# Kernel tuning notes

Measured on AMD Instinct MI355X. Metric: run time of the kernel, lower is better.

The kernel has to match this reference:

```python
import jax, jax.numpy as jnp
import numpy as np

NUM_HEADS = 8


def setup_inputs() -> dict:
    key = jax.random.key(0)
    ks = jax.random.split(key, 9)
    B, C, H, W = 2, 64, 48, 48
    Ck, Cv, Co = 64, 64, 64
    s = lambda fan_in: 1.0 / np.sqrt(fan_in)
    return {
        "x": jax.random.normal(ks[0], (B, C, H, W), jnp.float32),
        "Wq": jax.random.normal(ks[1], (Ck, C), jnp.float32) * s(C),
        "bq": jnp.zeros((Ck,), jnp.float32),
        "Wk": jax.random.normal(ks[2], (Ck, C), jnp.float32) * s(C),
        "bk": jnp.zeros((Ck,), jnp.float32),
        "Wv": jax.random.normal(ks[3], (Cv, C), jnp.float32) * s(C),
        "bv": jnp.zeros((Cv,), jnp.float32),
        "Wo": jax.random.normal(ks[4], (Co, Cv), jnp.float32) * s(Cv),
        "bo": jnp.zeros((Co,), jnp.float32),
    }


def _conv1x1(x, W, b):
    # 1x1 conv == channel matmul: [B,C,H,W] x [O,C] -> [B,O,H,W]
    return jnp.einsum("oc,bchw->bohw", W, x) + b[None, :, None, None]


def reference(x, Wq, bq, Wk, bk, Wv, bv, Wo, bo):
    B, _, H, W_ = x.shape
    nh = NUM_HEADS
    Ck, Cv = Wq.shape[0], Wv.shape[0]
    d = Ck // nh
    L = H * W_

    # NOTE: original torch code scales q in place via a view, so returned q is scaled.
    q = _conv1x1(x, Wq, bq) * (d ** -0.5)
    k = _conv1x1(x, Wk, bk)
    v = _conv1x1(x, Wv, bv)

    qs = q.reshape(B, nh, d, L)          # [B,h,d,Lq]
    ks = k.reshape(B, nh, d, L)          # [B,h,d,Lk]
    vs = v.reshape(B, nh, Cv // nh, L)   # [B,h,dv,Lk]

    logits = jnp.einsum("bhdq,bhdk->bhqk", qs, ks)   # [B,h,Lq,Lk]
    # softmax over the QUERY axis (dim=2), as in the original nn.Softmax(dim=2)
    weights = jax.nn.softmax(logits, axis=2)
    o = jnp.einsum("bhck,bhqk->bhcq", vs, weights)   # [B,h,dv,Lq]

    o = o.reshape(B, Cv, H, W_)
    out = _conv1x1(o, Wo, bo)
    return out, q
```

## Files before the change

kernel.cpp:

```cpp
#include <hip/hip_runtime.h>

#define LL   2304
#define CCH  64
#define NHD  8

static constexpr float QSCALE = 0.35355339059327373f;
static constexpr float LOG2E  = 1.4426950408889634f;

typedef _Float16 half2_t  __attribute__((ext_vector_type(2)));
typedef _Float16 half4_t  __attribute__((ext_vector_type(4)));
typedef _Float16 half8_t  __attribute__((ext_vector_type(8)));
typedef float    float16_t __attribute__((ext_vector_type(16)));

__device__ __forceinline__ half2_t pk_f16(float a, float b) {
    return __builtin_bit_cast(half2_t, __builtin_amdgcn_cvt_pkrtz(a, b));
}


__global__ __launch_bounds__(256) void k_qkv(
    const float* __restrict__ x,
    const float* __restrict__ Wq, const float* __restrict__ bq,
    const float* __restrict__ Wk, const float* __restrict__ bk,
    const float* __restrict__ Wv, const float* __restrict__ bv,
    float* __restrict__ qout,
    _Float16* __restrict__ Qt, _Float16* __restrict__ Kt, _Float16* __restrict__ Vt)
{
    __shared__ float xs[64][32];
    __shared__ float wsm[64][64];
    const int t   = threadIdx.x;
    const int l0  = blockIdx.x * 32;
    const int b   = blockIdx.y;
    const int mat = blockIdx.z;
    const float* W    = (mat == 0) ? Wq : (mat == 1 ? Wk : Wv);
    const float* bias = (mat == 0) ? bq : (mat == 1 ? bk : bv);
    const float* xb = x + (long)b * CCH * LL;

    #pragma unroll
    for (int p = 0; p < 2; ++p) {
        int flat = (p * 256 + t) * 4;
        int c = flat >> 5, l = flat & 31;
        *(float4*)&xs[c][l] = *(const float4*)&xb[(long)c * LL + l0 + l];
    }
    #pragma unroll
    for (int p = 0; p < 4; ++p) {
        int flat = (p * 256 + t) * 4;
        int c = flat >> 6, l = flat & 63;
        *(float4*)&wsm[c][l] = *(const float4*)&W[flat];
    }
    __syncthreads();

    const int l  = t & 31;
    const int cg = t >> 5;
    float acc[8];
    #pragma unroll
    for (int j = 0; j < 8; ++j) acc[j] = 0.f;
    for (int cp = 0; cp < 64; ++cp) {
        float xv = xs[cp][l];
        #pragma unroll
        for (int j = 0; j < 8; ++j) acc[j] = fmaf(wsm[cg * 8 + j][cp], xv, acc[j]);
    }
    long row = (long)(b * NHD + cg) * LL + l0 + l;
    if (mat == 0) {
        half8_t pq;
        #pragma unroll
        for (int j = 0; j < 8; ++j) {
            float qv = (acc[j] + bias[cg * 8 + j]) * QSCALE;
            qout[((long)b * CCH + cg * 8 + j) * LL + l0 + l] = qv;
            pq[j] = (_Float16)(qv * LOG2E);
        }
        *(half8_t*)(Qt + row * 8) = pq;
    } else if (mat == 1) {
        half8_t pk;
        #pragma unroll
        for (int j = 0; j < 8; ++j) pk[j] = (_Float16)(acc[j] + bias[cg * 8 + j]);
        *(half8_t*)(Kt + row * 8) = pk;
    } else {
        half8_t pv;
        #pragma unroll
        for (int j = 0; j < 8; ++j) pv[j] = (_Float16)(acc[j] + bias[cg * 8 + j]);
        *(half8_t*)(Vt + row * 8) = pv;
    }
}

__global__ __launch_bounds__(256) void k_denom(
    const _Float16* __restrict__ Qt, const _Float16* __restrict__ Kt,
    const _Float16* __restrict__ Vt, _Float16* __restrict__ V2)
{
    __shared__ _Float16 lQ[2][2][256][4];
    __shared__ float Dp[4][32];
    __shared__ float rDs[32];
    const int t    = threadIdx.x;
    const int bh   = blockIdx.y;
    const int k0   = blockIdx.x * 32;
    const int lane = t & 63, w = t >> 6;
    const int half = lane >> 5, l31 = lane & 31;

    half4_t kA = *(const half4_t*)(Kt + ((long)bh * LL + k0 + l31) * 8 + half * 4);

    const float4* qbase = (const float4*)(Qt + (long)bh * LL * 8);
    float4 pre = qbase[t];
    *(float2*)&lQ[0][0][t][0] = make_float2(pre.x, pre.y);
    *(float2*)&lQ[0][1][t][0] = make_float2(pre.z, pre.w);
    __syncthreads();

    float16_t D0 = {}, D1 = {};
    for (int ch = 0; ch < 9; ++ch) {
        const int buf = ch & 1;
        if (ch + 1 < 9) pre = qbase[(ch + 1) * 256 + t];
        {
            half4_t qB = *(const half4_t*)&lQ[buf][half][(2 * w + 0) * 32 + l31][0];
            float16_t S = __builtin_amdgcn_mfma_f32_32x32x8f16(kA, qB, (float16_t){}, 0, 0, 0);
            #pragma unroll
            for (int r = 0; r < 16; ++r) D0[r] += __builtin_amdgcn_exp2f(S[r]);
        }
        {
            half4_t qB = *(const half4_t*)&lQ[buf][half][(2 * w + 1) * 32 + l31][0];
            float16_t S = __builtin_amdgcn_mfma_f32_32x32x8f16(kA, qB, (float16_t){}, 0, 0, 0);
            #pragma unroll
            for (int r = 0; r < 16; ++r) D1[r] += __builtin_amdgcn_exp2f(S[r]);
        }
        if (ch + 1 < 9) {
            const int nb = (ch + 1) & 1;
            *(float2*)&lQ[nb][0][t][0] = make_float2(pre.x, pre.y);
            *(float2*)&lQ[nb][1][t][0] = make_float2(pre.z, pre.w);
            __syncthreads();
        }
    }
    #pragma unroll
    for (int r = 0; r < 16; ++r) {
        float v = D0[r] + D1[r];
        v += __shfl_xor(v, 1);  v += __shfl_xor(v, 2);  v += __shfl_xor(v, 4);
        v += __shfl_xor(v, 8);  v += __shfl_xor(v, 16);
        D0[r] = v;
    }
    __syncthreads();
    if (l31 == 0) {
        #pragma unroll
        for (int r = 0; r < 16; ++r) {
            int row = (r & 3) + 8 * (r >> 2) + 4 * half;
            Dp[w][row] = D0[r];
        }
    }
    __syncthreads();
    if (t < 32) rDs[t] = 256.0f / (Dp[0][t] + Dp[1][t] + Dp[2][t] + Dp[3][t]);
    __syncthreads();
    {
        int kk = t >> 3, c = t & 7;
        float v = (float)Vt[((long)bh * LL + k0 + kk) * 8 + c];
        V2[((long)bh * 8 + c) * LL + k0 + kk] = (_Float16)(v * rDs[kk]);
    }
}

__global__ __launch_bounds__(256) void k_av(
    const _Float16* __restrict__ Qt, const _Float16* __restrict__ Kt,
    const _Float16* __restrict__ V2, float* __restrict__ ot)
{
    __shared__ _Float16 lK[2][2][128][4];
    __shared__ _Float16 lVt[2][8][136];
    const int t    = threadIdx.x;
    const int bh   = blockIdx.y;
    const int s    = blockIdx.z;
    const int b = bh >> 3, h = bh & 7;
    const int lane = t & 63, w = t >> 6;
    const int half = lane >> 5, l31 = lane & 31;
    const int q0   = blockIdx.x * 128 + w * 32;

    half4_t qB = *(const half4_t*)(Qt + ((long)bh * LL + q0 + l31) * 8 + half * 4);

    const long ks0 = (long)s * 384;
    const float4*   kbase = (const float4*)(Kt + ((long)bh * LL + ks0) * 8);
    const _Float16* vbase = V2 + (long)bh * 8 * LL + ks0;

    const int vc = (t - 128) >> 4, vj = (t - 128) & 15;
    float4 pre;
    if (t < 128) pre = kbase[t];
    else         pre = *(const float4*)(vbase + (long)vc * LL + vj * 8);

    if (t < 128) {
        *(float2*)&lK[0][0][t][0] = make_float2(pre.x, pre.y);
        *(float2*)&lK[0][1][t][0] = make_float2(pre.z, pre.w);
    } else {
        *(float4*)&lVt[0][vc][vj * 8] = pre;
    }
    __syncthreads();

    float16_t O0 = {}, O1 = {};
    const int cl = l31 & 7;
    for (int ch = 0; ch < 3; ++ch) {
        const int buf = ch & 1;
        if (ch + 1 < 3) {
            if (t < 128) pre = kbase[(ch + 1) * 128 + t];
            else         pre = *(const float4*)(vbase + (long)vc * LL + (ch + 1) * 128 + vj * 8);
        }
        #pragma unroll
        for (int T = 0; T < 4; ++T) {
            int kb = T * 32;
            half4_t kA = *(const half4_t*)&lK[buf][half][kb + l31][0];
            float16_t S = __builtin_amdgcn_mfma_f32_32x32x8f16(kA, qB, (float16_t){}, 0, 0, 0);
            #pragma unroll
            for (int g = 0; g < 4; ++g) {
                half2_t p0 = pk_f16(__builtin_amdgcn_exp2f(S[4 * g + 0]),
                                    __builtin_amdgcn_exp2f(S[4 * g + 1]));
                half2_t p1 = pk_f16(__builtin_amdgcn_exp2f(S[4 * g + 2]),
                                    __builtin_amdgcn_exp2f(S[4 * g + 3]));
                half4_t pB = __builtin_shufflevector(p0, p1, 0, 1, 2, 3);
                half4_t vA = *(const half4_t*)&lVt[buf][cl][kb + g * 8 + half * 4];
                if (T & 1) O1 = __builtin_amdgcn_mfma_f32_32x32x8f16(vA, pB, O1, 0, 0, 0);
                else       O0 = __builtin_amdgcn_mfma_f32_32x32x8f16(vA, pB, O0, 0, 0, 0);
            }
        }
        if (ch + 1 < 3) {
            const int nb = (ch + 1) & 1;
            if (t < 128) {
                *(float2*)&lK[nb][0][t][0] = make_float2(pre.x, pre.y);
                *(float2*)&lK[nb][1][t][0] = make_float2(pre.z, pre.w);
            } else {
                *(float4*)&lVt[nb][vc][vj * 8] = pre;
            }
            __syncthreads();
        }
    }
    float* otb = ot + (long)s * (2 * CCH * LL) + ((long)b * CCH + h * 8) * LL;
    #pragma unroll
    for (int r = 0; r < 4; ++r) {
        int c = r + 4 * half;
        otb[(long)c * LL + q0 + l31] = (O0[r] + O1[r]) * (1.0f / 256.0f);
    }
}

__global__ __launch_bounds__(256) void k_out(
    const float* __restrict__ ot, const float* __restrict__ Wo,
    const float* __restrict__ bo, float* __restrict__ out)
{
    __shared__ float os[64][32];
    __shared__ float wsm[64][64];
    const int t  = threadIdx.x;
    const int l0 = blockIdx.x * 32;
    const int b  = blockIdx.y;
    const long SLAB = 2 * CCH * (long)LL;
    const float* ob = ot + (long)b * CCH * LL;

    #pragma unroll
    for (int p = 0; p < 2; ++p) {
        int flat = (p * 256 + t) * 4;
        int cv = flat >> 5, l = flat & 31;
        long off = (long)cv * LL + l0 + l;
        float4 a = *(const float4*)&ob[off];
        #pragma unroll
        for (int s = 1; s < 6; ++s) {
            float4 bb = *(const float4*)&ob[s * SLAB + off];
            a.x += bb.x; a.y += bb.y; a.z += bb.z; a.w += bb.w;
        }
        *(float4*)&os[cv][l] = a;
    }
    #pragma unroll
    for (int p = 0; p < 4; ++p) {
        int flat = (p * 256 + t) * 4;
        int c = flat >> 6, l = flat & 63;
        *(float4*)&wsm[c][l] = *(const float4*)&Wo[flat];
    }
    __syncthreads();

    const int l  = t & 31;
    const int cg = t >> 5;
    float acc[8];
    #pragma unroll
    for (int j = 0; j < 8; ++j) acc[j] = 0.f;
    for (int cv = 0; cv < 64; ++cv) {
        float xv = os[cv][l];
        #pragma unroll
        for (int j = 0; j < 8; ++j) acc[j] = fmaf(wsm[cg * 8 + j][cv], xv, acc[j]);
    }
    #pragma unroll
    for (int j = 0; j < 8; ++j) {
        int co = cg * 8 + j;
        out[((long)b * CCH + co) * LL + l0 + l] = acc[j] + bo[co];
    }
}

extern "C" void kernel_launch(void* const* d_in, const int* in_sizes, int n_in,
                              void* d_out, int out_size, void* d_ws, size_t ws_size,
                              hipStream_t stream)
{
    const float* x  = (const float*)d_in[0];
    const float* Wq = (const float*)d_in[1];
    const float* bq = (const float*)d_in[2];
    const float* Wk = (const float*)d_in[3];
    const float* bk = (const float*)d_in[4];
    const float* Wv = (const float*)d_in[5];
    const float* bv = (const float*)d_in[6];
    const float* Wo = (const float*)d_in[7];
    const float* bo = (const float*)d_in[8];

    float* out  = (float*)d_out;
    float* qout = out + 294912;

    _Float16* Qt = (_Float16*)d_ws;
    _Float16* Kt = Qt + 294912;
    _Float16* Vt = Kt + 294912;
    _Float16* V2 = Vt + 294912;
    float*    ot = (float*)(V2 + 294912);

    k_qkv  <<<dim3(72, 2, 3),  256, 0, stream>>>(x, Wq, bq, Wk, bk, Wv, bv, qout, Qt, Kt, Vt);
    k_denom<<<dim3(72, 16),    256, 0, stream>>>(Qt, Kt, Vt, V2);
    k_av   <<<dim3(18, 16, 6), 256, 0, stream>>>(Qt, Kt, V2, ot);
    k_out  <<<dim3(72, 2),     256, 0, stream>>>(ot, Wo, bo, out);
}
```

Before: 113.0 us.

## Load Q/K/V fragments directly from global memory instead of LDS staging

Both the denominator and attention-value kernels drop their double-buffered shared-memory staging and the block-wide barriers. Each wave now reads its MFMA operand fragments straight from global memory, relying on L1/L2 caches since the per-head working set is small. This removes LDS traffic and __syncthreads stalls, but trades them for more uncoalesced, latency-exposed global loads. The accumulator alternation in k_av also changes from per-tile to per-group.

```diff
diff --git a/kernel.cpp b/kernel.cpp
--- a/kernel.cpp
+++ b/kernel.cpp
@@ -86,7 +86,6 @@
     const _Float16* __restrict__ Qt, const _Float16* __restrict__ Kt,
     const _Float16* __restrict__ Vt, _Float16* __restrict__ V2)
 {
-    __shared__ _Float16 lQ[2][2][256][4];
     __shared__ float Dp[4][32];
     __shared__ float rDs[32];
     const int t    = threadIdx.x;
@@ -97,33 +96,19 @@
 
     half4_t kA = *(const half4_t*)(Kt + ((long)bh * LL + k0 + l31) * 8 + half * 4);
 
-    const float4* qbase = (const float4*)(Qt + (long)bh * LL * 8);
-    float4 pre = qbase[t];
-    *(float2*)&lQ[0][0][t][0] = make_float2(pre.x, pre.y);
-    *(float2*)&lQ[0][1][t][0] = make_float2(pre.z, pre.w);
-    __syncthreads();
+    const _Float16* qb = Qt + ((long)bh * LL + w * 576 + l31) * 8 + half * 4;
 
     float16_t D0 = {}, D1 = {};
-    for (int ch = 0; ch < 9; ++ch) {
-        const int buf = ch & 1;
-        if (ch + 1 < 9) pre = qbase[(ch + 1) * 256 + t];
-        {
-            half4_t qB = *(const half4_t*)&lQ[buf][half][(2 * w + 0) * 32 + l31][0];
-            float16_t S = __builtin_amdgcn_mfma_f32_32x32x8f16(kA, qB, (float16_t){}, 0, 0, 0);
+    #pragma unroll 2
+    for (int qt = 0; qt < 18; ++qt) {
+        half4_t qB = *(const half4_t*)(qb + (long)qt * 32 * 8);
+        float16_t S = __builtin_amdgcn_mfma_f32_32x32x8f16(kA, qB, (float16_t){}, 0, 0, 0);
+        if (qt & 1) {
+            #pragma unroll
+            for (int r = 0; r < 16; ++r) D1[r] += __builtin_amdgcn_exp2f(S[r]);
+        } else {
             #pragma unroll
             for (int r = 0; r < 16; ++r) D0[r] += __builtin_amdgcn_exp2f(S[r]);
-        }
-        {
-            half4_t qB = *(const half4_t*)&lQ[buf][half][(2 * w + 1) * 32 + l31][0];
-            float16_t S = __builtin_amdgcn_mfma_f32_32x32x8f16(kA, qB, (float16_t){}, 0, 0, 0);
-            #pragma unroll
-            for (int r = 0; r < 16; ++r) D1[r] += __builtin_amdgcn_exp2f(S[r]);
-        }
-        if (ch + 1 < 9) {
-            const int nb = (ch + 1) & 1;
-            *(float2*)&lQ[nb][0][t][0] = make_float2(pre.x, pre.y);
-            *(float2*)&lQ[nb][1][t][0] = make_float2(pre.z, pre.w);
-            __syncthreads();
         }
     }
     #pragma unroll
@@ -133,7 +118,6 @@
         v += __shfl_xor(v, 8);  v += __shfl_xor(v, 16);
         D0[r] = v;
     }
-    __syncthreads();
     if (l31 == 0) {
         #pragma unroll
         for (int r = 0; r < 16; ++r) {
@@ -155,8 +139,6 @@
     const _Float16* __restrict__ Qt, const _Float16* __restrict__ Kt,
     const _Float16* __restrict__ V2, float* __restrict__ ot)
 {
-    __shared__ _Float16 lK[2][2][128][4];
-    __shared__ _Float16 lVt[2][8][136];
     const int t    = threadIdx.x;
     const int bh   = blockIdx.y;
     const int s    = blockIdx.z;
@@ -164,60 +146,32 @@
     const int lane = t & 63, w = t >> 6;
     const int half = lane >> 5, l31 = lane & 31;
     const int q0   = blockIdx.x * 128 + w * 32;
+    const int cl   = l31 & 7;
 
     half4_t qB = *(const half4_t*)(Qt + ((long)bh * LL + q0 + l31) * 8 + half * 4);
 
-    const long ks0 = (long)s * 384;
-    const float4*   kbase = (const float4*)(Kt + ((long)bh * LL + ks0) * 8);
-    const _Float16* vbase = V2 + (long)bh * 8 * LL + ks0;
-
-    const int vc = (t - 128) >> 4, vj = (t - 128) & 15;
-    float4 pre;
-    if (t < 128) pre = kbase[t];
-    else         pre = *(const float4*)(vbase + (long)vc * LL + vj * 8);
-
-    if (t < 128) {
-        *(float2*)&lK[0][0][t][0] = make_float2(pre.x, pre.y);
-        *(float2*)&lK[0][1][t][0] = make_float2(pre.z, pre.w);
-    } else {
-        *(float4*)&lVt[0][vc][vj * 8] = pre;
-    }
-    __syncthreads();
+    const _Float16* kp = Kt + ((long)bh * LL + s * 384 + l31) * 8 + half * 4;
+    const _Float16* vp = V2 + ((long)bh * 8 + cl) * LL + s * 384 + half * 4;
 
     float16_t O0 = {}, O1 = {};
-    const int cl = l31 & 7;
-    for (int ch = 0; ch < 3; ++ch) {
-        const int buf = ch & 1;
-        if (ch + 1 < 3) {
-            if (t < 128) pre = kbase[(ch + 1) * 128 + t];
-            else         pre = *(const float4*)(vbase + (long)vc * LL + (ch + 1) * 128 + vj * 8);
-        }
-        #pragma unroll
-        for (int T = 0; T < 4; ++T) {
-            int kb = T * 32;
-            half4_t kA = *(const half4_t*)&lK[buf][half][kb + l31][0];
-            float16_t S = __builtin_amdgcn_mfma_f32_32x32x8f16(kA, qB, (float16_t){}, 0, 0, 0);
-            #pragma unroll
-            for (int g = 0; g < 4; ++g) {
-                half2_t p0 = pk_f16(__builtin_amdgcn_exp2f(S[4 * g + 0]),
-                                    __builtin_amdgcn_exp2f(S[4 * g + 1]));
-                half2_t p1 = pk_f16(__builtin_amdgcn_exp2f(S[4 * g + 2]),
-                                    __builtin_amdgcn_exp2f(S[4 * g + 3]));
-                half4_t pB = __builtin_shufflevector(p0, p1, 0, 1, 2, 3);
-                half4_t vA = *(const half4_t*)&lVt[buf][cl][kb + g * 8 + half * 4];
-                if (T & 1) O1 = __builtin_amdgcn_mfma_f32_32x32x8f16(vA, pB, O1, 0, 0, 0);
-                else       O0 = __builtin_amdgcn_mfma_f32_32x32x8f16(vA, pB, O0, 0, 0, 0);
-            }
-        }
-        if (ch + 1 < 3) {
-            const int nb = (ch + 1) & 1;
-            if (t < 128) {
-                *(float2*)&lK[nb][0][t][0] = make_float2(pre.x, pre.y);
-                *(float2*)&lK[nb][1][t][0] = make_float2(pre.z, pre.w);
-            } else {
-                *(float4*)&lVt[nb][vc][vj * 8] = pre;
-            }
-            __syncthreads();
+    #pragma unroll 2
+    for (int kt = 0; kt < 12; ++kt) {
+        half4_t kA  = *(const half4_t*)(kp + (long)kt * 32 * 8);
+        half4_t vA0 = *(const half4_t*)(vp + kt * 32 + 0);
+        half4_t vA1 = *(const half4_t*)(vp + kt * 32 + 8);
+        half4_t vA2 = *(const half4_t*)(vp + kt * 32 + 16);
+        half4_t vA3 = *(const half4_t*)(vp + kt * 32 + 24);
+        float16_t S = __builtin_amdgcn_mfma_f32_32x32x8f16(kA, qB, (float16_t){}, 0, 0, 0);
+        #pragma unroll
+        for (int g = 0; g < 4; ++g) {
+            half2_t p0 = pk_f16(__builtin_amdgcn_exp2f(S[4 * g + 0]),
+                                __builtin_amdgcn_exp2f(S[4 * g + 1]));
+            half2_t p1 = pk_f16(__builtin_amdgcn_exp2f(S[4 * g + 2]),
+                                __builtin_amdgcn_exp2f(S[4 * g + 3]));
+            half4_t pB = __builtin_shufflevector(p0, p1, 0, 1, 2, 3);
+            half4_t vA = (g == 0) ? vA0 : (g == 1) ? vA1 : (g == 2) ? vA2 : vA3;
+            if (g & 1) O1 = __builtin_amdgcn_mfma_f32_32x32x8f16(vA, pB, O1, 0, 0, 0);
+            else       O0 = __builtin_amdgcn_mfma_f32_32x32x8f16(vA, pB, O0, 0, 0, 0);
         }
     }
     float* otb = ot + (long)s * (2 * CCH * LL) + ((long)b * CCH + h * 8) * LL;
```

Measured after the change: 140.5 us. 1.24x slower.
